# Kernel optimization log

Hardware: AMD Instinct MI355X
Metric: run time of the kernel (lower is better)

Reference implementation:

```python
import jax, jax.numpy as jnp
import numpy as np

B, H, W, C = 32, 56, 56, 384
WS, SS, NH = 7, 3, 12
HD = C // NH
SCALE = HD ** -0.5
N = WS * WS
NW = (H // WS) * (W // WS)
HIDDEN = 4 * C
EPS = 1e-5


def _rel_pos_index():
    coords = np.stack(np.meshgrid(np.arange(WS), np.arange(WS), indexing='ij')).reshape(2, -1)
    rel = coords[:, :, None] - coords[:, None, :]
    rel = rel.transpose(1, 2, 0).astype(np.int64)
    rel[..., 0] += WS - 1
    rel[..., 1] += WS - 1
    rel[..., 0] *= 2 * WS - 1
    return rel.sum(-1)  # [N, N]


def _attn_mask():
    img = np.zeros((H, W), dtype=np.float32)
    slices = (slice(0, -WS), slice(-WS, -SS), slice(-SS, None))
    cnt = 0
    for hs in slices:
        for ws_ in slices:
            img[hs, ws_] = cnt
            cnt += 1
    mw = img.reshape(H // WS, WS, W // WS, WS).transpose(0, 2, 1, 3).reshape(-1, N)  # [nW, N]
    am = mw[:, None, :] - mw[:, :, None]
    return np.where(am != 0, -100.0, 0.0).astype(np.float32)  # [nW, N, N]


REL_IDX = jnp.asarray(_rel_pos_index())
ATTN_MASK = jnp.asarray(_attn_mask())


def _ln(x, g, b):
    mu = x.mean(-1, keepdims=True)
    var = ((x - mu) ** 2).mean(-1, keepdims=True)
    return (x - mu) * jax.lax.rsqrt(var + EPS) * g + b


def setup_inputs() -> dict:
    key = jax.random.key(0)
    ks = jax.random.split(key, 16)
    s = 0.02
    return {
        'x': jax.random.normal(ks[0], (B, H * W, C), jnp.float32),
        'norm1_g': jnp.ones((C,), jnp.float32),
        'norm1_b': jnp.zeros((C,), jnp.float32),
        'qkv_w': jax.random.normal(ks[1], (C, 3 * C), jnp.float32) * s,
        'qkv_b': jnp.zeros((3 * C,), jnp.float32),
        'bias_table': jax.random.normal(ks[2], ((2 * WS - 1) ** 2, NH), jnp.float32) * s,
        'proj_w': jax.random.normal(ks[3], (C, C), jnp.float32) * s,
        'proj_b': jnp.zeros((C,), jnp.float32),
        'norm2_g': jnp.ones((C,), jnp.float32),
        'norm2_b': jnp.zeros((C,), jnp.float32),
        'fc1_w': jax.random.normal(ks[4], (C, HIDDEN), jnp.float32) * s,
        'fc1_b': jnp.zeros((HIDDEN,), jnp.float32),
        'fc2_w': jax.random.normal(ks[5], (HIDDEN, C), jnp.float32) * s,
        'fc2_b': jnp.zeros((C,), jnp.float32),
    }


def reference(x, norm1_g, norm1_b, qkv_w, qkv_b, bias_table, proj_w, proj_b,
              norm2_g, norm2_b, fc1_w, fc1_b, fc2_w, fc2_b):
    shortcut = x
    h = _ln(x, norm1_g, norm1_b).reshape(B, H, W, C)
    # cyclic shift
    h = jnp.roll(h, shift=(-SS, -SS), axis=(1, 2))
    # window partition -> [B*nW, N, C]
    hw = h.reshape(B, H // WS, WS, W // WS, WS, C).transpose(0, 1, 3, 2, 4, 5).reshape(-1, N, C)
    Bw = hw.shape[0]
    # qkv
    qkv = (hw @ qkv_w + qkv_b).reshape(Bw, N, 3, NH, HD).transpose(2, 0, 3, 1, 4)
    q, k, v = qkv[0] * SCALE, qkv[1], qkv[2]  # [Bw, NH, N, HD]
    attn = jnp.einsum('whnd,whmd->whnm', q, k)
    rel_bias = bias_table[REL_IDX.reshape(-1)].reshape(N, N, NH).transpose(2, 0, 1)
    attn = attn + rel_bias[None]
    # shift mask: [Bw] = [B, nW]
    attn = attn.reshape(B, NW, NH, N, N) + ATTN_MASK[None, :, None]
    attn = jax.nn.softmax(attn.reshape(Bw, NH, N, N), axis=-1)
    o = jnp.einsum('whnm,whmd->whnd', attn, v).transpose(0, 2, 1, 3).reshape(Bw, N, C)
    o = o @ proj_w + proj_b
    # window reverse + reverse shift
    o = o.reshape(B, H // WS, W // WS, WS, WS, C).transpose(0, 1, 3, 2, 4, 5).reshape(B, H, W, C)
    o = jnp.roll(o, shift=(SS, SS), axis=(1, 2)).reshape(B, H * W, C)
    x = shortcut + o
    # MLP
    m = _ln(x, norm2_g, norm2_b)
    m = jax.nn.gelu(m @ fc1_w + fc1_b, approximate=False)
    m = m @ fc2_w + fc2_b
    return x + m
```

## Files before the change

kernel.cpp:

```cpp
#include <hip/hip_runtime.h>
#include <hip/hip_bf16.h>
#include <cstdint>
#include <cstddef>

static constexpr int Bv  = 32;
static constexpr int Cv  = 384;
static constexpr int Nv  = 49;
static constexpr int Mv  = 32 * 64 * 49;
static constexpr float SCALEv = 0.17677669529663687f;

using bf16 = __hip_bfloat16;
typedef __bf16 bf16x8 __attribute__((ext_vector_type(8)));
typedef float  f32x4  __attribute__((ext_vector_type(4)));

__global__ __launch_bounds__(256)
void wt_kernel(const float* __restrict__ w, bf16* __restrict__ wt, int K, int N) {
    int idx = blockIdx.x * 256 + threadIdx.x;
    if (idx >= K * N) return;
    int n = idx / K, k = idx - n * K;
    wt[idx] = (bf16)w[(size_t)k * N + n];
}

__global__ __launch_bounds__(256)
void bm_kernel(const float* __restrict__ btab, float* __restrict__ bmt) {
    const int cls = blockIdx.x, h = blockIdx.y;
    for (int idx = threadIdx.x; idx < 4096; idx += 256) {
        int col = idx >> 6, row = idx & 63;
        float v;
        if (col >= 49) {
            v = -1e30f;
        } else {
            int n = row < 49 ? row : 48;
            int m = col;
            int i1 = n / 7, j1 = n - i1 * 7;
            int i2 = m / 7, j2 = m - i2 * 7;
            v = btab[((i1 - i2 + 6) * 13 + (j1 - j2 + 6)) * 12 + h];
            int lh1 = (cls & 2) ? (i1 < 4 ? 1 : 2) : 0;
            int lw1 = (cls & 1) ? (j1 < 4 ? 1 : 2) : 0;
            int lh2 = (cls & 2) ? (i2 < 4 ? 1 : 2) : 0;
            int lw2 = (cls & 1) ? (j2 < 4 ? 1 : 2) : 0;
            if ((lh1 * 3 + lw1) != (lh2 * 3 + lw2)) v += -100.f;
        }
        bmt[((size_t)(cls * 12 + h) * 64 + col) * 64 + row] = v;
    }
}

template <int MODE>
__global__ __launch_bounds__(256)
void ln_kernel(const float* __restrict__ src, const float* __restrict__ gam,
               const float* __restrict__ bet, bf16* __restrict__ dst) {
    const int wave = threadIdx.x >> 6, lane = threadIdx.x & 63;
    const int r = blockIdx.x * 4 + wave;
    size_t srow;
    if (MODE == 0) {
        int w  = r / 49, n = r - w * 49;
        int b  = w >> 6, win = w & 63;
        int hb = win >> 3, wb = win & 7;
        int ii = n / 7, jj = n - ii * 7;
        int hh = hb * 7 + ii + 3; if (hh >= 56) hh -= 56;
        int ww = wb * 7 + jj + 3; if (ww >= 56) ww -= 56;
        srow = (size_t)b * 3136 + hh * 56 + ww;
    } else {
        srow = (size_t)r;
    }
    const float* p = src + srow * 384;
    float vals[6];
    float s = 0.f, s2 = 0.f;
#pragma unroll
    for (int t = 0; t < 6; ++t) {
        float v = p[t * 64 + lane];
        vals[t] = v; s += v; s2 += v * v;
    }
#pragma unroll
    for (int o = 32; o > 0; o >>= 1) {
        s  += __shfl_xor(s,  o, 64);
        s2 += __shfl_xor(s2, o, 64);
    }
    const float mu  = s * (1.f / 384.f);
    const float var = s2 * (1.f / 384.f) - mu * mu;
    const float rs  = rsqrtf(var + 1e-5f);
    bf16* q = dst + (size_t)r * 384;
#pragma unroll
    for (int t = 0; t < 6; ++t) {
        int e = t * 64 + lane;
        q[e] = (bf16)((vals[t] - mu) * rs * gam[e] + bet[e]);
    }
}

__global__ __launch_bounds__(64)
void attn_kernel(const bf16* __restrict__ qkv, const float* __restrict__ bmt,
                 bf16* __restrict__ o) {
    const int w = blockIdx.x;
    const int h = blockIdx.y;
    const int lane = threadIdx.x;
    const int quad = lane >> 4, l16 = lane & 15;
    __shared__ bf16 Vt[32][72];
    __shared__ bf16 Ps[64][72];

    const size_t rowbase = (size_t)w * 49;

    for (int idx = lane; idx < 49 * 16; idx += 64) {
        int row = idx >> 4, dp = (idx & 15) << 1;
        const bf16* src = qkv + (rowbase + row) * 1152 + 768 + h * 32 + dp;
        Vt[dp][row]     = src[0];
        Vt[dp + 1][row] = src[1];
    }
    for (int idx = lane; idx < 512; idx += 64) {
        int d = idx >> 4, c = idx & 15;
        if (c) Vt[d][48 + c] = (bf16)0.f;
    }

    f32x4 acc[4][4] = {};
    bf16x8 af[4], bfr[4];
#pragma unroll
    for (int i = 0; i < 4; ++i) {
        int row = 16 * i + l16; if (row > 48) row = 48;
        af[i] = *(const bf16x8*)(qkv + (rowbase + row) * 1152 + h * 32 + quad * 8);
    }
#pragma unroll
    for (int j = 0; j < 4; ++j) {
        int row = 16 * j + l16; if (row > 48) row = 48;
        bfr[j] = *(const bf16x8*)(qkv + (rowbase + row) * 1152 + 384 + h * 32 + quad * 8);
    }
#pragma unroll
    for (int i = 0; i < 4; ++i)
#pragma unroll
        for (int j = 0; j < 4; ++j)
            acc[i][j] = __builtin_amdgcn_mfma_f32_16x16x32_bf16(af[i], bfr[j], acc[i][j], 0, 0, 0);

    const int cls = (((w & 63) >= 56) ? 2 : 0) + (((w & 7) == 7) ? 1 : 0);
    const float* bmbase = bmt + (size_t)(cls * 12 + h) * 4096;
    float inv[4][4];
#pragma unroll
    for (int i = 0; i < 4; ++i) {
        f32x4 bm[4];
#pragma unroll
        for (int j = 0; j < 4; ++j)
            bm[j] = *(const f32x4*)(bmbase + (16 * j + l16) * 64 + 16 * i + quad * 4);
#pragma unroll
        for (int t = 0; t < 4; ++t) {
            float v0 = acc[i][0][t] + bm[0][t];
            float v1 = acc[i][1][t] + bm[1][t];
            float v2 = acc[i][2][t] + bm[2][t];
            float v3 = acc[i][3][t] + bm[3][t];
            float mx = fmaxf(fmaxf(v0, v1), fmaxf(v2, v3));
#pragma unroll
            for (int ofs = 1; ofs < 16; ofs <<= 1) mx = fmaxf(mx, __shfl_xor(mx, ofs, 64));
            float p0 = __expf(v0 - mx), p1 = __expf(v1 - mx);
            float p2 = __expf(v2 - mx), p3 = __expf(v3 - mx);
            float s = (p0 + p1) + (p2 + p3);
#pragma unroll
            for (int ofs = 1; ofs < 16; ofs <<= 1) s += __shfl_xor(s, ofs, 64);
            inv[i][t] = 1.f / s;
            int prow = 16 * i + quad * 4 + t;
            Ps[prow][l16]      = (bf16)p0;
            Ps[prow][16 + l16] = (bf16)p1;
            Ps[prow][32 + l16] = (bf16)p2;
            Ps[prow][48 + l16] = (bf16)p3;
        }
    }
    __syncthreads();

    f32x4 oacc[4][2] = {};
    bf16x8 vb[2][2];
#pragma unroll
    for (int jn = 0; jn < 2; ++jn)
#pragma unroll
        for (int ks = 0; ks < 2; ++ks)
            vb[jn][ks] = *(const bf16x8*)(&Vt[16 * jn + l16][32 * ks + quad * 8]);
#pragma unroll
    for (int i = 0; i < 4; ++i) {
#pragma unroll
        for (int ks = 0; ks < 2; ++ks) {
            bf16x8 pa = *(const bf16x8*)(&Ps[16 * i + l16][32 * ks + quad * 8]);
#pragma unroll
            for (int jn = 0; jn < 2; ++jn)
                oacc[i][jn] = __builtin_amdgcn_mfma_f32_16x16x32_bf16(pa, vb[jn][ks], oacc[i][jn], 0, 0, 0);
        }
    }

#pragma unroll
    for (int i = 0; i < 4; ++i) {
        int nbase = 16 * i + quad * 4;
#pragma unroll
        for (int t = 0; t < 4; ++t) {
            int n = nbase + t;
            if (n < 49) {
                bf16* dst = o + (rowbase + n) * 384 + h * 32;
                dst[l16]      = (bf16)(oacc[i][0][t] * inv[i][t]);
                dst[16 + l16] = (bf16)(oacc[i][1][t] * inv[i][t]);
            }
        }
    }
}

template <int EPI>
__global__ __launch_bounds__(256)
void gemm_bt(const bf16* __restrict__ A, const bf16* __restrict__ Bt,
             const float* __restrict__ bias, int N, int K,
             bf16* __restrict__ outb, float* __restrict__ outf,
             const float* __restrict__ resid) {
    __shared__ bf16 As[128 * 64];
    __shared__ bf16 Bs[128 * 64];
    const int tid  = threadIdx.x;
    const int lane = tid & 63, wave = tid >> 6;
    const int quad = lane >> 4, l16 = lane & 15;
    const int wm = wave >> 1, wn = wave & 1;
    const long m0 = (long)blockIdx.y * 128;
    const long n0 = (long)blockIdx.x * 128;

    f32x4 acc[4][4] = {};

    for (int k0 = 0; k0 < K; k0 += 64) {
        __syncthreads();
#pragma unroll
        for (int it = 0; it < 4; ++it) {
            int e = it * 256 + tid;
            int row = e >> 3;
            int col = (e & 7) << 3;
            __builtin_amdgcn_global_load_lds(
                (const __attribute__((address_space(1))) unsigned int*)(A + (size_t)(m0 + row) * K + k0 + col),
                (__attribute__((address_space(3))) unsigned int*)(As + (size_t)e * 8),
                16, 0, 0);
            __builtin_amdgcn_global_load_lds(
                (const __attribute__((address_space(1))) unsigned int*)(Bt + (size_t)(n0 + row) * K + k0 + col),
                (__attribute__((address_space(3))) unsigned int*)(Bs + (size_t)e * 8),
                16, 0, 0);
        }
        __syncthreads();
#pragma unroll
        for (int kk = 0; kk < 64; kk += 32) {
            bf16x8 af[4], bfr[4];
#pragma unroll
            for (int i = 0; i < 4; ++i)
                af[i] = *(const bf16x8*)(As + (wm * 64 + i * 16 + l16) * 64 + kk + quad * 8);
#pragma unroll
            for (int j = 0; j < 4; ++j)
                bfr[j] = *(const bf16x8*)(Bs + (wn * 64 + j * 16 + l16) * 64 + kk + quad * 8);
#pragma unroll
            for (int i = 0; i < 4; ++i)
#pragma unroll
                for (int j = 0; j < 4; ++j)
                    acc[i][j] = __builtin_amdgcn_mfma_f32_16x16x32_bf16(af[i], bfr[j], acc[i][j], 0, 0, 0);
        }
    }

#pragma unroll
    for (int i = 0; i < 4; ++i) {
        const long mbase = m0 + wm * 64 + i * 16 + quad * 4;
#pragma unroll
        for (int j = 0; j < 4; ++j) {
            const int col = (int)n0 + wn * 64 + j * 16 + l16;
            const float bv = bias[col];
            f32x4 r = acc[i][j];
#pragma unroll
            for (int t = 0; t < 4; ++t) {
                const long m = mbase + t;
                float val = r[t] + bv;
                if constexpr (EPI == 0) {
                    float sc = (col < 384) ? SCALEv : 1.0f;
                    outb[(size_t)m * N + col] = (bf16)(val * sc);
                } else if constexpr (EPI == 1) {
                    int w  = (int)(m / 49), n = (int)(m - (long)w * 49);
                    int b  = w >> 6, win = w & 63;
                    int hb = win >> 3, wb = win & 7;
                    int ii = n / 7, jj = n - ii * 7;
                    int hh = hb * 7 + ii + 3; if (hh >= 56) hh -= 56;
                    int ww = wb * 7 + jj + 3; if (ww >= 56) ww -= 56;
                    size_t dst = ((size_t)b * 3136 + hh * 56 + ww) * 384 + col;
                    outf[dst] = resid[dst] + val;
                } else if constexpr (EPI == 2) {
                    float g = 0.5f * val * (1.0f + erff(val * 0.70710678118654752f));
                    outb[(size_t)m * N + col] = (bf16)g;
                } else {
                    size_t oo = (size_t)m * N + col;
                    outf[oo] = resid[oo] + val;
                }
            }
        }
    }
}

extern "C" void kernel_launch(void* const* d_in, const int* in_sizes, int n_in,
                              void* d_out, int out_size, void* d_ws, size_t ws_size,
                              hipStream_t stream) {
    const float* x     = (const float*)d_in[0];
    const float* n1g   = (const float*)d_in[1];
    const float* n1b   = (const float*)d_in[2];
    const float* qkvw  = (const float*)d_in[3];
    const float* qkvb  = (const float*)d_in[4];
    const float* btab  = (const float*)d_in[5];
    const float* projw = (const float*)d_in[6];
    const float* projb = (const float*)d_in[7];
    const float* n2g   = (const float*)d_in[8];
    const float* n2b   = (const float*)d_in[9];
    const float* fc1w  = (const float*)d_in[10];
    const float* fc1b  = (const float*)d_in[11];
    const float* fc2w  = (const float*)d_in[12];
    const float* fc2b  = (const float*)d_in[13];
    float* out = (float*)d_out;

    char* ws = (char*)d_ws;
    size_t off = 0;
    auto take = [&](size_t bytes) {
        char* p = ws + off;
        off += (bytes + 255) & ~(size_t)255;
        return p;
    };
    bf16* qkv_wt  = (bf16*)take((size_t)1152 * 384 * 2);
    bf16* proj_wt = (bf16*)take((size_t)384 * 384 * 2);
    bf16* fc1_wt  = (bf16*)take((size_t)1536 * 384 * 2);
    bf16* fc2_wt  = (bf16*)take((size_t)384 * 1536 * 2);
    float* bmt    = (float*)take((size_t)4 * 12 * 64 * 64 * 4);
    bf16* qkv_buf = (bf16*)take((size_t)Mv * 1152 * 2);
    bf16* o_buf   = (bf16*)take((size_t)Mv * 384 * 2);
    bf16* hw_buf  = (bf16*)take((size_t)Mv * 384 * 2);
    float* x1     = (float*)take((size_t)Mv * 384 * 4);
    bf16* g_buf   = qkv_buf;
    bf16* x1n     = hw_buf;

    wt_kernel<<<(384 * 1152 + 255) / 256, 256, 0, stream>>>(qkvw,  qkv_wt,  384, 1152);
    wt_kernel<<<(384 * 384  + 255) / 256, 256, 0, stream>>>(projw, proj_wt, 384, 384);
    wt_kernel<<<(384 * 1536 + 255) / 256, 256, 0, stream>>>(fc1w,  fc1_wt,  384, 1536);
    wt_kernel<<<(1536 * 384 + 255) / 256, 256, 0, stream>>>(fc2w,  fc2_wt,  1536, 384);
    bm_kernel<<<dim3(4, 12), 256, 0, stream>>>(btab, bmt);
    ln_kernel<0><<<Mv / 4, 256, 0, stream>>>(x, n1g, n1b, hw_buf);
    gemm_bt<0><<<dim3(1152 / 128, Mv / 128), 256, 0, stream>>>(
        hw_buf, qkv_wt, qkvb, 1152, 384, qkv_buf, nullptr, nullptr);
    attn_kernel<<<dim3(2048, 12), 64, 0, stream>>>(qkv_buf, bmt, o_buf);
    gemm_bt<1><<<dim3(384 / 128, Mv / 128), 256, 0, stream>>>(
        o_buf, proj_wt, projb, 384, 384, nullptr, x1, x);
    ln_kernel<1><<<Mv / 4, 256, 0, stream>>>(x1, n2g, n2b, x1n);
    gemm_bt<2><<<dim3(1536 / 128, Mv / 128), 256, 0, stream>>>(
        x1n, fc1_wt, fc1b, 1536, 384, g_buf, nullptr, nullptr);
    gemm_bt<3><<<dim3(384 / 128, Mv / 128), 256, 0, stream>>>(
        g_buf, fc2_wt, fc2b, 384, 1536, nullptr, out, x1);
}
```

Before: 1.324 ms.

## Double-buffer GEMM LDS tiles and remap workgroups across XCDs

Splits the GEMM shared-memory A/B tiles into two buffers so the next K-tile's global-to-LDS loads are issued before the MFMA work on the current tile, overlapping load latency with compute and removing one barrier per iteration. It also remaps the block index so consecutive tiles are grouped by XCD (ord&7), aiming for better L2 reuse on the multi-die GPU. LDS use doubles to 64 KB per block, which may reduce occupancy. The remap assumes the workgroup count divides by 8.

```diff
diff --git a/kernel.cpp b/kernel.cpp
--- a/kernel.cpp
+++ b/kernel.cpp
@@ -200,19 +200,27 @@
              const float* __restrict__ bias, int N, int K,
              bf16* __restrict__ outb, float* __restrict__ outf,
              const float* __restrict__ resid) {
-    __shared__ bf16 As[128 * 64];
-    __shared__ bf16 Bs[128 * 64];
+    __shared__ bf16 As[2][128 * 64];
+    __shared__ bf16 Bs[2][128 * 64];
     const int tid  = threadIdx.x;
     const int lane = tid & 63, wave = tid >> 6;
     const int quad = lane >> 4, l16 = lane & 15;
     const int wm = wave >> 1, wn = wave & 1;
-    const long m0 = (long)blockIdx.y * 128;
-    const long n0 = (long)blockIdx.x * 128;
+
+    const int nbx = gridDim.x;
+    const int nwg = nbx * (int)gridDim.y;
+    const int ord = (int)blockIdx.y * nbx + (int)blockIdx.x;
+    const int cpx = nwg >> 3;
+    const int work = (ord & 7) * cpx + (ord >> 3);
+    const int by = work / nbx;
+    const int bx = work - by * nbx;
+    const long m0 = (long)by * 128;
+    const long n0 = (long)bx * 128;
 
     f32x4 acc[4][4] = {};
-
-    for (int k0 = 0; k0 < K; k0 += 64) {
-        __syncthreads();
+    const int nk = K >> 6;
+
+    auto stage = [&](int buf, int k0) {
 #pragma unroll
         for (int it = 0; it < 4; ++it) {
             int e = it * 256 + tid;
@@ -220,29 +228,40 @@
             int col = (e & 7) << 3;
             __builtin_amdgcn_global_load_lds(
                 (const __attribute__((address_space(1))) unsigned int*)(A + (size_t)(m0 + row) * K + k0 + col),
-                (__attribute__((address_space(3))) unsigned int*)(As + (size_t)e * 8),
+                (__attribute__((address_space(3))) unsigned int*)(&As[buf][(size_t)e * 8]),
                 16, 0, 0);
             __builtin_amdgcn_global_load_lds(
                 (const __attribute__((address_space(1))) unsigned int*)(Bt + (size_t)(n0 + row) * K + k0 + col),
-                (__attribute__((address_space(3))) unsigned int*)(Bs + (size_t)e * 8),
+                (__attribute__((address_space(3))) unsigned int*)(&Bs[buf][(size_t)e * 8]),
                 16, 0, 0);
         }
-        __syncthreads();
+    };
+
+    stage(0, 0);
+    __syncthreads();
+
+    int cur = 0;
+    for (int kt = 0; kt < nk; ++kt) {
+        if (kt + 1 < nk) stage(cur ^ 1, (kt + 1) * 64);
+        const bf16* Ap = As[cur];
+        const bf16* Bp = Bs[cur];
 #pragma unroll
         for (int kk = 0; kk < 64; kk += 32) {
             bf16x8 af[4], bfr[4];
 #pragma unroll
             for (int i = 0; i < 4; ++i)
-                af[i] = *(const bf16x8*)(As + (wm * 64 + i * 16 + l16) * 64 + kk + quad * 8);
+                af[i] = *(const bf16x8*)(Ap + (wm * 64 + i * 16 + l16) * 64 + kk + quad * 8);
 #pragma unroll
             for (int j = 0; j < 4; ++j)
-                bfr[j] = *(const bf16x8*)(Bs + (wn * 64 + j * 16 + l16) * 64 + kk + quad * 8);
+                bfr[j] = *(const bf16x8*)(Bp + (wn * 64 + j * 16 + l16) * 64 + kk + quad * 8);
 #pragma unroll
             for (int i = 0; i < 4; ++i)
 #pragma unroll
                 for (int j = 0; j < 4; ++j)
                     acc[i][j] = __builtin_amdgcn_mfma_f32_16x16x32_bf16(af[i], bfr[j], acc[i][j], 0, 0, 0);
         }
+        __syncthreads();
+        cur ^= 1;
     }
 
 #pragma unroll
```

Result: no change. 1.319 ms (-0.4%).
